# Optimization experiments

Hardware: AMD Instinct MI355X
Metric: run time of the kernel (lower is better)

## Reference

```python
import jax, jax.numpy as jnp
import numpy as np

N_NODES = 1_000_000
N_EDGES = 16_000_000


def setup_inputs() -> dict:
    key = jax.random.key(0)
    ks = jax.random.split(key, 12)
    feat = jax.random.normal(ks[0], (N_NODES, 1), dtype=jnp.float32)
    # symmetric GCN norm D^{-1/2}; positive values in (0, 1]
    norm = jax.random.uniform(ks[1], (N_NODES, 1), dtype=jnp.float32, minval=0.05, maxval=1.0)
    src = jax.random.randint(ks[2], (N_EDGES,), 0, N_NODES, dtype=jnp.int32)
    dst = jax.random.randint(ks[3], (N_EDGES,), 0, N_NODES, dtype=jnp.int32)
    dims = [(1, 3), (3, 3), (3, 3), (3, 3), (3, 3), (3, 1)]
    params = {}
    for i, (fi, fo) in enumerate(dims):
        w = jax.random.normal(ks[4 + i], (fi, fo), dtype=jnp.float32) * (1.0 / np.sqrt(fi))
        params[f"W{i+1}"] = w
        params[f"b{i+1}"] = jnp.zeros((fo,), dtype=jnp.float32)
    return dict(feat=feat, norm=norm, src=src, dst=dst, **params)


def _gcn_layer(h, norm, W, b, src, dst, n_nodes):
    # DGL-style GraphConv with symmetric norm:
    #   h = h * norm; agg_i = sum_{(j->i) in E} h_j; h = agg * norm; h = h @ W + b; relu
    h = h * norm                                   # [N, F]
    msgs = jnp.take(h, src, axis=0)                # [E, F] irregular gather
    agg = jax.ops.segment_sum(msgs, dst, num_segments=n_nodes)  # [N, F] scatter-add
    agg = agg * norm
    return jax.nn.relu(agg @ W + b)


def reference(feat, norm, W1, b1, W2, b2, W3, b3, W4, b4, W5, b5, W6, b6, src, dst):
    n = feat.shape[0]
    h = feat
    for W, b in ((W1, b1), (W2, b2), (W3, b3), (W4, b4), (W5, b5), (W6, b6)):
        h = _gcn_layer(h, norm, W, b, src, dst, n)
    return h  # [N, 1]
```

## Files before the change

kernel.cpp:

```cpp
#include <hip/hip_runtime.h>

#ifndef __HIP_PLATFORM_AMD__
#define unsafeAtomicAdd atomicAdd
#endif


#define BT 256
#define NBLK 256
#define BSHIFT 12
#define BSIZE 4096
#define LMASK 4095
#define SSH 18
#define NBINS 1024
#define M (NBLK * NBINS)
#define BTL 1024

__device__ __forceinline__ int edge_key(int s, int d) {
  return ((d >> BSHIFT) << 2) | (s >> SSH);
}

__global__ void k_init(const float* __restrict__ feat, const float* __restrict__ norm,
                       float* __restrict__ s0, int N) {
  int i = blockIdx.x * BT + threadIdx.x;
  if (i < N) s0[i] = feat[i] * norm[i];
}

__global__ void k_zero3(float* __restrict__ a0, float* __restrict__ a1,
                        float* __restrict__ a2, int N) {
  int i = blockIdx.x * BT + threadIdx.x;
  if (i < N) { a0[i] = 0.0f; a1[i] = 0.0f; a2[i] = 0.0f; }
}

__global__ void k_phist(const int* __restrict__ src, const int* __restrict__ dst,
                        int* __restrict__ histB, int E, int chunk) {
  __shared__ int h[NBINS];
  for (int i = threadIdx.x; i < NBINS; i += BT) h[i] = 0;
  __syncthreads();
  int b = blockIdx.x;
  int beg = b * chunk, end = min(beg + chunk, E);
  int i = beg + (int)threadIdx.x * 4;
  for (; i + 3 < end; i += BT * 4) {
    int4 u = *(const int4*)(src + i);
    int4 v = *(const int4*)(dst + i);
    atomicAdd(&h[edge_key(u.x, v.x)], 1);
    atomicAdd(&h[edge_key(u.y, v.y)], 1);
    atomicAdd(&h[edge_key(u.z, v.z)], 1);
    atomicAdd(&h[edge_key(u.w, v.w)], 1);
  }
  for (; i < end; ++i) atomicAdd(&h[edge_key(src[i], dst[i])], 1);
  __syncthreads();
  for (int k = threadIdx.x; k < NBINS; k += BT) histB[b * NBINS + k] = h[k];
}

__global__ void k_transp(const int* __restrict__ in, int* __restrict__ out, int R, int C) {
  __shared__ int tile[64][65];
  int c0 = blockIdx.x * 64, r0 = blockIdx.y * 64;
  int tx = threadIdx.x & 63, ty = threadIdx.x >> 6;
  for (int j = 0; j < 16; ++j) {
    int r = ty + j * 4;
    tile[r][tx] = in[(r0 + r) * C + c0 + tx];
  }
  __syncthreads();
  for (int j = 0; j < 16; ++j) {
    int r = ty + j * 4;
    out[(c0 + r) * R + r0 + tx] = tile[tx][r];
  }
}

__global__ void k_blockSum(const int* __restrict__ data, int* __restrict__ partial, int Mlen) {
  __shared__ int tmp[BT];
  int i = blockIdx.x * BT + threadIdx.x;
  tmp[threadIdx.x] = (i < Mlen) ? data[i] : 0;
  __syncthreads();
  for (int off = BT / 2; off > 0; off >>= 1) {
    if (threadIdx.x < off) tmp[threadIdx.x] += tmp[threadIdx.x + off];
    __syncthreads();
  }
  if (threadIdx.x == 0) partial[blockIdx.x] = tmp[0];
}

__global__ void k_scanPartials(int* __restrict__ partial, int nb) {
  __shared__ int tmp[BT];
  __shared__ int carry;
  int t = threadIdx.x;
  if (t == 0) carry = 0;
  __syncthreads();
  for (int base = 0; base < nb; base += BT) {
    int i = base + t;
    int v = (i < nb) ? partial[i] : 0;
    tmp[t] = v;
    __syncthreads();
    for (int off = 1; off < BT; off <<= 1) {
      int x = 0;
      if (t >= off) x = tmp[t - off];
      __syncthreads();
      tmp[t] += x;
      __syncthreads();
    }
    if (i < nb) partial[i] = tmp[t] - v + carry;
    __syncthreads();
    if (t == BT - 1) carry += tmp[BT - 1];
    __syncthreads();
  }
}

__global__ void k_scanFinal(int* __restrict__ data, const int* __restrict__ partial, int Mlen) {
  __shared__ int tmp[BT];
  int t = threadIdx.x;
  int i = blockIdx.x * BT + t;
  int v = (i < Mlen) ? data[i] : 0;
  tmp[t] = v;
  __syncthreads();
  for (int off = 1; off < BT; off <<= 1) {
    int x = 0;
    if (t >= off) x = tmp[t - off];
    __syncthreads();
    tmp[t] += x;
    __syncthreads();
  }
  if (i < Mlen) data[i] = tmp[t] - v + partial[blockIdx.x];
}

__global__ void k_pscatter(const int* __restrict__ src, const int* __restrict__ dst,
                           const int* __restrict__ scanT, unsigned int* __restrict__ packed,
                           int E, int chunk) {
  __shared__ int cur[NBINS];
  int b = blockIdx.x;
  for (int k = threadIdx.x; k < NBINS; k += BT) cur[k] = scanT[b * NBINS + k];
  __syncthreads();
  int beg = b * chunk, end = min(beg + chunk, E);
  int i = beg + (int)threadIdx.x * 4;
  for (; i + 3 < end; i += BT * 4) {
    int4 u = *(const int4*)(src + i);
    int4 v = *(const int4*)(dst + i);
    int p;
    p = atomicAdd(&cur[edge_key(u.x, v.x)], 1);
    packed[p] = ((unsigned)u.x << BSHIFT) | (unsigned)(v.x & LMASK);
    p = atomicAdd(&cur[edge_key(u.y, v.y)], 1);
    packed[p] = ((unsigned)u.y << BSHIFT) | (unsigned)(v.y & LMASK);
    p = atomicAdd(&cur[edge_key(u.z, v.z)], 1);
    packed[p] = ((unsigned)u.z << BSHIFT) | (unsigned)(v.z & LMASK);
    p = atomicAdd(&cur[edge_key(u.w, v.w)], 1);
    packed[p] = ((unsigned)u.w << BSHIFT) | (unsigned)(v.w & LMASK);
  }
  for (; i < end; ++i) {
    int p = atomicAdd(&cur[edge_key(src[i], dst[i])], 1);
    packed[p] = ((unsigned)src[i] << BSHIFT) | (unsigned)(dst[i] & LMASK);
  }
}


#define ACC3(p)                                             \
  {                                                         \
    unsigned pp = (p);                                      \
    float4 m = ((const float4*)sPrev)[pp >> BSHIFT];        \
    int loc = pp & LMASK;                                   \
    atomicAdd(&a0[loc], m.x);                               \
    atomicAdd(&a1[loc], m.y);                               \
    atomicAdd(&a2[loc], m.z);                               \
  }

#define ACC1(p)                                             \
  {                                                         \
    unsigned pp = (p);                                      \
    atomicAdd(&a[pp & LMASK], sIn[pp >> BSHIFT]);           \
  }

__global__ __launch_bounds__(BTL) void k_edge3p(
    const int* __restrict__ scanT, const unsigned int* __restrict__ packed,
    const float* __restrict__ sPrev, float* __restrict__ agg0,
    float* __restrict__ agg1, float* __restrict__ agg2, int N) {
  __shared__ float a0[BSIZE], a1[BSIZE], a2[BSIZE];
  int k = blockIdx.x >> 1, h = blockIdx.x & 1;
  for (int i = threadIdx.x; i < BSIZE; i += BTL) { a0[i] = 0.0f; a1[i] = 0.0f; a2[i] = 0.0f; }
  int bbeg = scanT[k << 2], bend = scanT[(k << 2) + 4];
  int mid = bbeg + ((bend - bbeg) >> 1);
  int beg = h ? mid : bbeg;
  int end = h ? bend : mid;
  __syncthreads();
  int abeg = min(end, (beg + 3) & ~3);
  {
    int t = beg + (int)threadIdx.x;
    if (t < abeg) ACC3(packed[t]);
  }
  int i = abeg + (int)threadIdx.x * 8;
  for (; i + 7 < end; i += BTL * 8) {
    uint4 pa = *(const uint4*)(packed + i);
    uint4 pb = *(const uint4*)(packed + i + 4);
    float4 m0 = ((const float4*)sPrev)[pa.x >> BSHIFT];
    float4 m1 = ((const float4*)sPrev)[pa.y >> BSHIFT];
    float4 m2 = ((const float4*)sPrev)[pa.z >> BSHIFT];
    float4 m3 = ((const float4*)sPrev)[pa.w >> BSHIFT];
    float4 m4 = ((const float4*)sPrev)[pb.x >> BSHIFT];
    float4 m5 = ((const float4*)sPrev)[pb.y >> BSHIFT];
    float4 m6 = ((const float4*)sPrev)[pb.z >> BSHIFT];
    float4 m7 = ((const float4*)sPrev)[pb.w >> BSHIFT];
    atomicAdd(&a0[pa.x & LMASK], m0.x); atomicAdd(&a1[pa.x & LMASK], m0.y); atomicAdd(&a2[pa.x & LMASK], m0.z);
    atomicAdd(&a0[pa.y & LMASK], m1.x); atomicAdd(&a1[pa.y & LMASK], m1.y); atomicAdd(&a2[pa.y & LMASK], m1.z);
    atomicAdd(&a0[pa.z & LMASK], m2.x); atomicAdd(&a1[pa.z & LMASK], m2.y); atomicAdd(&a2[pa.z & LMASK], m2.z);
    atomicAdd(&a0[pa.w & LMASK], m3.x); atomicAdd(&a1[pa.w & LMASK], m3.y); atomicAdd(&a2[pa.w & LMASK], m3.z);
    atomicAdd(&a0[pb.x & LMASK], m4.x); atomicAdd(&a1[pb.x & LMASK], m4.y); atomicAdd(&a2[pb.x & LMASK], m4.z);
    atomicAdd(&a0[pb.y & LMASK], m5.x); atomicAdd(&a1[pb.y & LMASK], m5.y); atomicAdd(&a2[pb.y & LMASK], m5.z);
    atomicAdd(&a0[pb.z & LMASK], m6.x); atomicAdd(&a1[pb.z & LMASK], m6.y); atomicAdd(&a2[pb.z & LMASK], m6.z);
    atomicAdd(&a0[pb.w & LMASK], m7.x); atomicAdd(&a1[pb.w & LMASK], m7.y); atomicAdd(&a2[pb.w & LMASK], m7.z);
  }
  for (; i < end; ++i) ACC3(packed[i]);
  __syncthreads();
  int node0 = k << BSHIFT;
  for (int t = threadIdx.x; t < BSIZE; t += BTL) {
    int node = node0 + t;
    if (node < N) {
      unsafeAtomicAdd(&agg0[node], a0[t]);
      unsafeAtomicAdd(&agg1[node], a1[t]);
      unsafeAtomicAdd(&agg2[node], a2[t]);
    }
  }
}

__global__ __launch_bounds__(BTL) void k_edge1p(
    const int* __restrict__ scanT, const unsigned int* __restrict__ packed,
    const float* __restrict__ sIn, float* __restrict__ agg0, int N) {
  __shared__ float a[BSIZE];
  int k = blockIdx.x >> 1, h = blockIdx.x & 1;
  for (int i = threadIdx.x; i < BSIZE; i += BTL) a[i] = 0.0f;
  int bbeg = scanT[k << 2], bend = scanT[(k << 2) + 4];
  int mid = bbeg + ((bend - bbeg) >> 1);
  int beg = h ? mid : bbeg;
  int end = h ? bend : mid;
  __syncthreads();
  int abeg = min(end, (beg + 3) & ~3);
  {
    int t = beg + (int)threadIdx.x;
    if (t < abeg) ACC1(packed[t]);
  }
  int i = abeg + (int)threadIdx.x * 8;
  for (; i + 7 < end; i += BTL * 8) {
    uint4 pa = *(const uint4*)(packed + i);
    uint4 pb = *(const uint4*)(packed + i + 4);
    float m0 = sIn[pa.x >> BSHIFT];
    float m1 = sIn[pa.y >> BSHIFT];
    float m2 = sIn[pa.z >> BSHIFT];
    float m3 = sIn[pa.w >> BSHIFT];
    float m4 = sIn[pb.x >> BSHIFT];
    float m5 = sIn[pb.y >> BSHIFT];
    float m6 = sIn[pb.z >> BSHIFT];
    float m7 = sIn[pb.w >> BSHIFT];
    atomicAdd(&a[pa.x & LMASK], m0);
    atomicAdd(&a[pa.y & LMASK], m1);
    atomicAdd(&a[pa.z & LMASK], m2);
    atomicAdd(&a[pa.w & LMASK], m3);
    atomicAdd(&a[pb.x & LMASK], m4);
    atomicAdd(&a[pb.y & LMASK], m5);
    atomicAdd(&a[pb.z & LMASK], m6);
    atomicAdd(&a[pb.w & LMASK], m7);
  }
  for (; i < end; ++i) ACC1(packed[i]);
  __syncthreads();
  int node0 = k << BSHIFT;
  for (int t = threadIdx.x; t < BSIZE; t += BTL) {
    int node = node0 + t;
    if (node < N) unsafeAtomicAdd(&agg0[node], a[t]);
  }
}


__global__ void k_node12(const float* __restrict__ norm, const float* __restrict__ W1,
                         const float* __restrict__ b1, float* __restrict__ agg0,
                         float* __restrict__ sA, int N) {
  int i = blockIdx.x * BT + threadIdx.x;
  if (i >= N) return;
  float n = norm[i];
  float pre = agg0[i] * n;
  agg0[i] = 0.0f;
  float h0 = fmaxf(0.0f, pre * W1[0] + b1[0]);
  float h1 = fmaxf(0.0f, pre * W1[1] + b1[1]);
  float h2 = fmaxf(0.0f, pre * W1[2] + b1[2]);
  ((float4*)sA)[i] = make_float4(h0 * n, h1 * n, h2 * n, 0.0f);
}

__global__ void k_node33(const float* __restrict__ norm, const float* __restrict__ W,
                         const float* __restrict__ bias, float* __restrict__ agg0,
                         float* __restrict__ agg1, float* __restrict__ agg2,
                         float* __restrict__ sNext, int N) {
  int i = blockIdx.x * BT + threadIdx.x;
  if (i >= N) return;
  float n = norm[i];
  float x0 = agg0[i] * n, x1 = agg1[i] * n, x2 = agg2[i] * n;
  agg0[i] = 0.0f; agg1[i] = 0.0f; agg2[i] = 0.0f;
  float h0 = fmaxf(0.0f, x0 * W[0] + x1 * W[3] + x2 * W[6] + bias[0]);
  float h1 = fmaxf(0.0f, x0 * W[1] + x1 * W[4] + x2 * W[7] + bias[1]);
  float h2 = fmaxf(0.0f, x0 * W[2] + x1 * W[5] + x2 * W[8] + bias[2]);
  ((float4*)sNext)[i] = make_float4(h0 * n, h1 * n, h2 * n, 0.0f);
}

__global__ void k_node56(const float* __restrict__ norm, const float* __restrict__ W5,
                         const float* __restrict__ b5, const float* __restrict__ W6,
                         float* __restrict__ agg0, float* __restrict__ agg1,
                         float* __restrict__ agg2, float* __restrict__ sB, int N) {
  int i = blockIdx.x * BT + threadIdx.x;
  if (i >= N) return;
  float n = norm[i];
  float x0 = agg0[i] * n, x1 = agg1[i] * n, x2 = agg2[i] * n;
  agg0[i] = 0.0f; agg1[i] = 0.0f; agg2[i] = 0.0f;
  float h0 = fmaxf(0.0f, x0 * W5[0] + x1 * W5[3] + x2 * W5[6] + b5[0]);
  float h1 = fmaxf(0.0f, x0 * W5[1] + x1 * W5[4] + x2 * W5[7] + b5[1]);
  float h2 = fmaxf(0.0f, x0 * W5[2] + x1 * W5[5] + x2 * W5[8] + b5[2]);
  sB[i] = (h0 * W6[0] + h1 * W6[1] + h2 * W6[2]) * n;
}

__global__ void k_final(const float* __restrict__ norm, const float* __restrict__ b6,
                        const float* __restrict__ agg0, float* __restrict__ out, int N) {
  int i = blockIdx.x * BT + threadIdx.x;
  if (i >= N) return;
  out[i] = fmaxf(0.0f, agg0[i] * norm[i] + b6[0]);
}

extern "C" void kernel_launch(void* const* d_in, const int* in_sizes, int n_in,
                              void* d_out, int out_size, void* d_ws, size_t ws_size,
                              hipStream_t stream) {
  const float* feat = (const float*)d_in[0];
  const float* norm = (const float*)d_in[1];
  const int* src = (const int*)d_in[2];
  const int* dst = (const int*)d_in[3];
  const float* W1 = (const float*)d_in[4];
  const float* b1 = (const float*)d_in[5];
  const float* W2 = (const float*)d_in[6];
  const float* b2 = (const float*)d_in[7];
  const float* W3 = (const float*)d_in[8];
  const float* b3 = (const float*)d_in[9];
  const float* W4 = (const float*)d_in[10];
  const float* b4 = (const float*)d_in[11];
  const float* W5 = (const float*)d_in[12];
  const float* b5 = (const float*)d_in[13];
  const float* W6 = (const float*)d_in[14];
  const float* b6 = (const float*)d_in[15];
  float* out = (float*)d_out;

  const int N = in_sizes[0];
  const int E = in_sizes[2];
  const int nbNode = (N + BT - 1) / BT;
  const int nBkt = (N + BSIZE - 1) >> BSHIFT;
  const int chunk = (((E + NBLK - 1) / NBLK) + 3) & ~3;

  unsigned int* packed = (unsigned int*)d_ws;
  int* histB = (int*)(packed + (size_t)E);
  int* histT = histB + (size_t)M;
  int* scanT = histT + (size_t)M;
  int* partial = scanT + (size_t)M;
  float* s0B = (float*)(partial + M / BT);
  float* sA = s0B + (size_t)N;
  float* sA2 = sA + (size_t)4 * N;
  float* agg0 = sA2 + (size_t)4 * N;
  float* agg1 = agg0 + (size_t)N;
  float* agg2 = agg1 + (size_t)N;

  k_init<<<nbNode, BT, 0, stream>>>(feat, norm, s0B, N);
  k_zero3<<<nbNode, BT, 0, stream>>>(agg0, agg1, agg2, N);
  k_phist<<<NBLK, BT, 0, stream>>>(src, dst, histB, E, chunk);
  {
    dim3 g1(NBINS / 64, NBLK / 64);
    k_transp<<<g1, BT, 0, stream>>>(histB, histT, NBLK, NBINS);
  }
  k_blockSum<<<M / BT, BT, 0, stream>>>(histT, partial, M);
  k_scanPartials<<<1, BT, 0, stream>>>(partial, M / BT);
  k_scanFinal<<<M / BT, BT, 0, stream>>>(histT, partial, M);
  {
    dim3 g2(NBLK / 64, NBINS / 64);
    k_transp<<<g2, BT, 0, stream>>>(histT, scanT, NBINS, NBLK);
  }
  k_pscatter<<<NBLK, BT, 0, stream>>>(src, dst, scanT, packed, E, chunk);

  const int gEdge = nBkt * 2;

  k_edge1p<<<gEdge, BTL, 0, stream>>>(scanT, packed, s0B, agg0, N);
  k_node12<<<nbNode, BT, 0, stream>>>(norm, W1, b1, agg0, sA, N);

  k_edge3p<<<gEdge, BTL, 0, stream>>>(scanT, packed, sA, agg0, agg1, agg2, N);
  k_node33<<<nbNode, BT, 0, stream>>>(norm, W2, b2, agg0, agg1, agg2, sA2, N);

  k_edge3p<<<gEdge, BTL, 0, stream>>>(scanT, packed, sA2, agg0, agg1, agg2, N);
  k_node33<<<nbNode, BT, 0, stream>>>(norm, W3, b3, agg0, agg1, agg2, sA, N);

  k_edge3p<<<gEdge, BTL, 0, stream>>>(scanT, packed, sA, agg0, agg1, agg2, N);
  k_node33<<<nbNode, BT, 0, stream>>>(norm, W4, b4, agg0, agg1, agg2, sA2, N);

  k_edge3p<<<gEdge, BTL, 0, stream>>>(scanT, packed, sA2, agg0, agg1, agg2, N);
  k_node56<<<nbNode, BT, 0, stream>>>(norm, W5, b5, W6, agg0, agg1, agg2, s0B, N);

  k_edge1p<<<gEdge, BTL, 0, stream>>>(scanT, packed, s0B, agg0, N);
  k_final<<<nbNode, BT, 0, stream>>>(norm, b6, agg0, out, N);
}
```

Measured before the change: 1.599 ms.

## Split edge aggregation into four source-range phases for gather cache locality

Each edge aggregation kernel is launched four times, once per source-index sub-bin (src>>18), so that each phase gathers from only a quarter of the node feature array, which is meant to improve L2/MALL hit rates for the irregular gather. The flush to global memory now skips zero partial sums to reduce global atomics. The cost is four times as many launches, four times the shared-memory zeroing and flush passes, and more global atomics overall, because each node is flushed up to four times.

```diff
diff --git a/kernel.cpp b/kernel.cpp
--- a/kernel.cpp
+++ b/kernel.cpp
@@ -166,14 +166,14 @@
     atomicAdd(&a[pp & LMASK], sIn[pp >> BSHIFT]);           \
   }
 
-__global__ __launch_bounds__(BTL) void k_edge3p(
+__global__ __launch_bounds__(BTL) void k_edge3ph(
     const int* __restrict__ scanT, const unsigned int* __restrict__ packed,
     const float* __restrict__ sPrev, float* __restrict__ agg0,
-    float* __restrict__ agg1, float* __restrict__ agg2, int N) {
+    float* __restrict__ agg1, float* __restrict__ agg2, int N, int phase) {
   __shared__ float a0[BSIZE], a1[BSIZE], a2[BSIZE];
   int k = blockIdx.x >> 1, h = blockIdx.x & 1;
   for (int i = threadIdx.x; i < BSIZE; i += BTL) { a0[i] = 0.0f; a1[i] = 0.0f; a2[i] = 0.0f; }
-  int bbeg = scanT[k << 2], bend = scanT[(k << 2) + 4];
+  int bbeg = scanT[(k << 2) + phase], bend = scanT[(k << 2) + phase + 1];
   int mid = bbeg + ((bend - bbeg) >> 1);
   int beg = h ? mid : bbeg;
   int end = h ? bend : mid;
@@ -210,20 +210,21 @@
   for (int t = threadIdx.x; t < BSIZE; t += BTL) {
     int node = node0 + t;
     if (node < N) {
-      unsafeAtomicAdd(&agg0[node], a0[t]);
-      unsafeAtomicAdd(&agg1[node], a1[t]);
-      unsafeAtomicAdd(&agg2[node], a2[t]);
+      float v0 = a0[t], v1 = a1[t], v2 = a2[t];
+      if (v0 != 0.0f) unsafeAtomicAdd(&agg0[node], v0);
+      if (v1 != 0.0f) unsafeAtomicAdd(&agg1[node], v1);
+      if (v2 != 0.0f) unsafeAtomicAdd(&agg2[node], v2);
     }
   }
 }
 
-__global__ __launch_bounds__(BTL) void k_edge1p(
+__global__ __launch_bounds__(BTL) void k_edge1ph(
     const int* __restrict__ scanT, const unsigned int* __restrict__ packed,
-    const float* __restrict__ sIn, float* __restrict__ agg0, int N) {
+    const float* __restrict__ sIn, float* __restrict__ agg0, int N, int phase) {
   __shared__ float a[BSIZE];
   int k = blockIdx.x >> 1, h = blockIdx.x & 1;
   for (int i = threadIdx.x; i < BSIZE; i += BTL) a[i] = 0.0f;
-  int bbeg = scanT[k << 2], bend = scanT[(k << 2) + 4];
+  int bbeg = scanT[(k << 2) + phase], bend = scanT[(k << 2) + phase + 1];
   int mid = bbeg + ((bend - bbeg) >> 1);
   int beg = h ? mid : bbeg;
   int end = h ? bend : mid;
@@ -259,7 +260,10 @@
   int node0 = k << BSHIFT;
   for (int t = threadIdx.x; t < BSIZE; t += BTL) {
     int node = node0 + t;
-    if (node < N) unsafeAtomicAdd(&agg0[node], a[t]);
+    if (node < N) {
+      float v = a[t];
+      if (v != 0.0f) unsafeAtomicAdd(&agg0[node], v);
+    }
   }
 }
 
@@ -372,21 +376,27 @@
 
   const int gEdge = nBkt * 2;
 
-  k_edge1p<<<gEdge, BTL, 0, stream>>>(scanT, packed, s0B, agg0, N);
+  for (int p = 0; p < 4; ++p)
+    k_edge1ph<<<gEdge, BTL, 0, stream>>>(scanT, packed, s0B, agg0, N, p);
   k_node12<<<nbNode, BT, 0, stream>>>(norm, W1, b1, agg0, sA, N);
 
-  k_edge3p<<<gEdge, BTL, 0, stream>>>(scanT, packed, sA, agg0, agg1, agg2, N);
+  for (int p = 0; p < 4; ++p)
+    k_edge3ph<<<gEdge, BTL, 0, stream>>>(scanT, packed, sA, agg0, agg1, agg2, N, p);
   k_node33<<<nbNode, BT, 0, stream>>>(norm, W2, b2, agg0, agg1, agg2, sA2, N);
 
-  k_edge3p<<<gEdge, BTL, 0, stream>>>(scanT, packed, sA2, agg0, agg1, agg2, N);
+  for (int p = 0; p < 4; ++p)
+    k_edge3ph<<<gEdge, BTL, 0, stream>>>(scanT, packed, sA2, agg0, agg1, agg2, N, p);
   k_node33<<<nbNode, BT, 0, stream>>>(norm, W3, b3, agg0, agg1, agg2, sA, N);
 
-  k_edge3p<<<gEdge, BTL, 0, stream>>>(scanT, packed, sA, agg0, agg1, agg2, N);
+  for (int p = 0; p < 4; ++p)
+    k_edge3ph<<<gEdge, BTL, 0, stream>>>(scanT, packed, sA, agg0, agg1, agg2, N, p);
   k_node33<<<nbNode, BT, 0, stream>>>(norm, W4, b4, agg0, agg1, agg2, sA2, N);
 
-  k_edge3p<<<gEdge, BTL, 0, stream>>>(scanT, packed, sA2, agg0, agg1, agg2, N);
+  for (int p = 0; p < 4; ++p)
+    k_edge3ph<<<gEdge, BTL, 0, stream>>>(scanT, packed, sA2, agg0, agg1, agg2, N, p);
   k_node56<<<nbNode, BT, 0, stream>>>(norm, W5, b5, W6, agg0, agg1, agg2, s0B, N);
 
-  k_edge1p<<<gEdge, BTL, 0, stream>>>(scanT, packed, s0B, agg0, N);
+  for (int p = 0; p < 4; ++p)
+    k_edge1ph<<<gEdge, BTL, 0, stream>>>(scanT, packed, s0B, agg0, N, p);
   k_final<<<nbNode, BT, 0, stream>>>(norm, b6, agg0, out, N);
 }
```

New measurement: 1.747 ms. 9.3% more time.
